# Kernel tuning notes

Hardware: AMD Instinct MI355X
Metric: run time of the kernel (lower is better)

## Reference

```python
import jax, jax.numpy as jnp
import numpy as np

B, N, FEAT, HID, CTX = 16384, 7, 512, 256, 256
COMB = N * HID + CTX  # 2048


def setup_inputs() -> dict:
    key = jax.random.key(0)
    ks = jax.random.split(key, 20)
    s = lambda k, shape, sc=0.05: jax.random.normal(k, shape, dtype=jnp.float32) * sc
    adj = jax.random.randint(ks[1], (N, N), 0, 2).astype(jnp.float32)
    # guarantee self-loops so no row is fully masked (still exercise nan_to_num path robustly)
    adj = jnp.maximum(adj, jnp.eye(N, dtype=jnp.float32))
    return {
        "node_feats": jax.random.normal(ks[0], (B, N, FEAT), dtype=jnp.float32),
        "adj": adj,
        "context": jax.random.normal(ks[2], (B, CTX), dtype=jnp.float32),
        "base_preds": jax.random.normal(ks[3], (B, 5), dtype=jnp.float32),
        "W1": s(ks[4], (HID, FEAT)),
        "a1": s(ks[5], (1, 2 * HID)),
        "W2": s(ks[6], (HID, HID)),
        "a2": s(ks[7], (1, 2 * HID)),
        "wh1_w": s(ks[8], (32, COMB)), "wh1_b": s(ks[9], (32,)),
        "wh2_w": s(ks[10], (16, 32)), "wh2_b": s(ks[11], (16,)),
        "wh3_w": s(ks[12], (5, 16)), "wh3_b": s(ks[13], (5,)),
        "rh1_w": s(ks[14], (16, COMB)), "rh1_b": s(ks[15], (16,)),
        "rh2_w": s(ks[16], (1, 16)), "rh2_b": s(ks[17], (1,)),
    }


def _gat_layer(x, adj, W, a):
    # x: (B, N, in_dim); W: (D, in_dim); a: (1, 2D)
    h = jnp.einsum('bni,di->bnd', x, W)  # (B, N, D)
    D = W.shape[0]
    # a([h_i, h_j]) == h_i @ a[:, :D] + h_j @ a[:, D:]
    s_i = h @ a[0, :D]   # (B, N)
    s_j = h @ a[0, D:]   # (B, N)
    e = s_i[:, :, None] + s_j[:, None, :]          # (B, N, N)
    e = jax.nn.leaky_relu(e, negative_slope=0.2)
    e = jnp.where(adj[None] == 0, -jnp.inf, e)
    alpha = jax.nn.softmax(e, axis=-1)
    alpha = jnp.nan_to_num(alpha, nan=0.0)
    out = jnp.einsum('bij,bjd->bid', alpha, h)     # (B, N, D)
    return out, alpha


def reference(node_feats, adj, context, base_preds, W1, a1, W2, a2,
              wh1_w, wh1_b, wh2_w, wh2_b, wh3_w, wh3_b,
              rh1_w, rh1_b, rh2_w, rh2_b):
    h, _attn1 = _gat_layer(node_feats, adj, W1, a1)
    h = jax.nn.relu(h)
    h, attn2 = _gat_layer(h, adj, W2, a2)
    h = jax.nn.relu(h)
    graph_embed = h.reshape(h.shape[0], -1)                 # (B, N*D)
    combined = jnp.concatenate([graph_embed, context], -1)  # (B, COMB)
    # weight head (dropout is inference-mode identity)
    t = jax.nn.relu(combined @ wh1_w.T + wh1_b)
    t = jax.nn.relu(t @ wh2_w.T + wh2_b)
    raw_weights = t @ wh3_w.T + wh3_b                       # (B, 5)
    weights = jax.nn.softmax(raw_weights, axis=-1)
    weighted_pred = jnp.sum(weights * base_preds, axis=-1)  # (B,)
    r = jnp.tanh(combined @ rh1_w.T + rh1_b)
    residual = (r @ rh2_w.T + rh2_b)[:, 0] * 0.05
    pred = jnp.maximum(weighted_pred + residual, 0.05)
    return pred, weights, attn2
```

## Files before the change

kernel.cpp:

```cpp
#include <hip/hip_runtime.h>

#define B_SZ 16384
#define NN 7
#define HID 256
#define COMB 2048

typedef __attribute__((ext_vector_type(8))) short short8;
typedef __attribute__((ext_vector_type(4))) float floatx4;
typedef __attribute__((ext_vector_type(4))) unsigned short ushortx4;
typedef unsigned short us;

__device__ __forceinline__ float bf2f(us u) {
    union { unsigned int i; float f; } v; v.i = ((unsigned int)u) << 16; return v.f;
}
__device__ __forceinline__ us f2bf(float f) {
    union { unsigned int i; float f; } v; v.f = f;
    return (us)((v.i + 0x7FFFu + ((v.i >> 16) & 1u)) >> 16);
}
__device__ __forceinline__ us f2bf_fast(float f) {
    union { unsigned int i; float f; } v; v.f = f;
    return (us)((v.i + 0x8000u) >> 16);
}

__device__ __forceinline__ int hoff(int r, int k8) {
    return ((r >> 3) << 8) | ((r & 7) << 5) | (k8 & 24) | ((k8 ^ r) & 7);
}
__device__ __forceinline__ int aoff(int r, int k8) {
    return ((r >> 3) << 6) | ((r & 7) << 3) | ((k8 ^ r) & 7);
}

__global__ __launch_bounds__(256) void pack_weights(const float* __restrict__ W1,
                                                    const float* __restrict__ W2,
                                                    const float* __restrict__ wh1,
                                                    const float* __restrict__ rh1,
                                                    us* __restrict__ dst) {
    int i = (blockIdx.x * 256 + threadIdx.x) * 4;
    if (i >= 294912) return;
    const float* src; int off;
    if (i < 131072)      { src = W1;  off = i; }
    else if (i < 196608) { src = W2;  off = i - 131072; }
    else if (i < 262144) { src = wh1; off = i - 196608; }
    else                 { src = rh1; off = i - 262144; }
    floatx4 v = *(const floatx4*)(src + off);
    ushortx4 o = {f2bf(v[0]), f2bf(v[1]), f2bf(v[2]), f2bf(v[3])};
    *(ushortx4*)(dst + i) = o;
}

template <bool WRITE_ALPHA>
__device__ __forceinline__ void attn_graph(us* hs, int r0, const float* adjs, const float* avec,
                                           float* alpha_dst, int lane) {
    const int k8 = lane >> 1, sub = (lane & 1) * 4;
    float hv[NN][4];
#pragma unroll
    for (int n = 0; n < NN; ++n) {
        ushortx4 rr = *(const ushortx4*)(hs + hoff(r0 + n, k8) * 8 + sub);
        hv[n][0] = bf2f(rr[0]); hv[n][1] = bf2f(rr[1]);
        hv[n][2] = bf2f(rr[2]); hv[n][3] = bf2f(rr[3]);
    }
    floatx4 ai = *(const floatx4*)(avec + lane * 4);
    floatx4 aj = *(const floatx4*)(avec + HID + lane * 4);
    float si[NN], sj[NN];
#pragma unroll
    for (int n = 0; n < NN; ++n) {
        float pi = hv[n][0] * ai[0] + hv[n][1] * ai[1] + hv[n][2] * ai[2] + hv[n][3] * ai[3];
        float pj = hv[n][0] * aj[0] + hv[n][1] * aj[1] + hv[n][2] * aj[2] + hv[n][3] * aj[3];
#pragma unroll
        for (int off = 32; off; off >>= 1) {
            pi += __shfl_xor(pi, off);
            pj += __shfl_xor(pj, off);
        }
        si[n] = pi; sj[n] = pj;
    }
    const int j = lane & 7;
    float sjm = sj[0];
    if (j == 1) sjm = sj[1];
    if (j == 2) sjm = sj[2];
    if (j == 3) sjm = sj[3];
    if (j == 4) sjm = sj[4];
    if (j == 5) sjm = sj[5];
    if (j == 6) sjm = sj[6];
    const int jc = (j < 7) ? j : 0;
    float alpha[NN];
#pragma unroll
    for (int i = 0; i < NN; ++i) {
        float x = si[i] + sjm;
        x = (x >= 0.f) ? x : 0.2f * x;
        bool ok = (j < 7) && (adjs[i * 7 + jc] != 0.f);
        float e = ok ? x : -1e30f;
        float m = e;
        m = fmaxf(m, __shfl_xor(m, 1, 8));
        m = fmaxf(m, __shfl_xor(m, 2, 8));
        m = fmaxf(m, __shfl_xor(m, 4, 8));
        float ex = ok ? __expf(e - m) : 0.f;
        float s = ex;
        s += __shfl_xor(s, 1, 8);
        s += __shfl_xor(s, 2, 8);
        s += __shfl_xor(s, 4, 8);
        alpha[i] = (s > 0.f) ? ex * __frcp_rn(s) : 0.f;
    }
    if (WRITE_ALPHA && lane < 7) {
#pragma unroll
        for (int i = 0; i < NN; ++i) alpha_dst[i * NN + lane] = alpha[i];
    }
#pragma unroll
    for (int i = 0; i < NN; ++i) {
        floatx4 o = (floatx4){0.f, 0.f, 0.f, 0.f};
#pragma unroll
        for (int jj = 0; jj < NN; ++jj) {
            float a = __shfl(alpha[i], jj, 8);
            o[0] += a * hv[jj][0]; o[1] += a * hv[jj][1];
            o[2] += a * hv[jj][2]; o[3] += a * hv[jj][3];
        }
        ushortx4 st = {f2bf(fmaxf(o[0], 0.f)), f2bf(fmaxf(o[1], 0.f)),
                       f2bf(fmaxf(o[2], 0.f)), f2bf(fmaxf(o[3], 0.f))};
        *(ushortx4*)(hs + hoff(r0 + i, k8) * 8 + sub) = st;
    }
}

__device__ __forceinline__ void cwrite(us* hs, floatx4 (&acc)[4][2], int wave, int quad, int m16) {
#pragma unroll
    for (int rt = 0; rt < 4; ++rt)
#pragma unroll
        for (int ct = 0; ct < 2; ++ct)
#pragma unroll
            for (int i = 0; i < 4; ++i) {
                int row = rt * 16 + quad * 4 + i;
                if (row < 56)
                    hs[hoff(row, wave * 4 + ct * 2 + (m16 >> 3)) * 8 + (m16 & 7)] =
                        f2bf(acc[rt][ct][i]);
            }
}

__global__ __launch_bounds__(512, 4) void fused_all(
    const float* __restrict__ Af, const us* __restrict__ W1b, const us* __restrict__ W2b,
    const us* __restrict__ Whb, const float* __restrict__ adj, const float* __restrict__ a1v,
    const float* __restrict__ a2v, const float* __restrict__ context,
    const float* __restrict__ wh1_b, const float* __restrict__ wh2_w,
    const float* __restrict__ wh2_b, const float* __restrict__ wh3_w,
    const float* __restrict__ wh3_b, const float* __restrict__ rh1_b,
    const float* __restrict__ rh2_w, const float* __restrict__ rh2_b,
    const float* __restrict__ base_preds, float* __restrict__ out) {
    __shared__ __attribute__((aligned(16))) us hs[16384];
    __shared__ __attribute__((aligned(16))) char ubuf[16384];
    __shared__ float adjs[52];
    us* As = (us*)ubuf;
    float* red = (float*)ubuf;
    float* fin = red + 3072;
    const int tid = threadIdx.x;
    const int wave = tid >> 6, lane = tid & 63;
    const int quad = lane >> 4, m16 = lane & 15;
    const long gbase = (long)blockIdx.x * 8;
    if (tid < 49) adjs[tid] = adj[tid];
    *(ushortx4*)(hs + 14336 + tid * 4) = (ushortx4){0, 0, 0, 0};

    floatx4 acc[4][2];
#pragma unroll
    for (int rt = 0; rt < 4; ++rt)
#pragma unroll
        for (int ct = 0; ct < 2; ++ct) acc[rt][ct] = (floatx4){0.f, 0.f, 0.f, 0.f};

    const int r = tid >> 3, kq8 = tid & 7;
    long rowA = gbase * 7 + r; if (rowA > 114687) rowA = 114687;
    const float* aptr = Af + rowA * 512 + kq8 * 8;
    us* wdst = As + aoff(r, kq8) * 8;
    const int colb = wave * 32;

    floatx4 v0 = *(const floatx4*)aptr;
    floatx4 v1 = *(const floatx4*)(aptr + 4);
#pragma unroll
    for (int s = 0; s < 8; ++s) {
        short8 sv;
        sv[0] = f2bf_fast(v0[0]); sv[1] = f2bf_fast(v0[1]);
        sv[2] = f2bf_fast(v0[2]); sv[3] = f2bf_fast(v0[3]);
        sv[4] = f2bf_fast(v1[0]); sv[5] = f2bf_fast(v1[1]);
        sv[6] = f2bf_fast(v1[2]); sv[7] = f2bf_fast(v1[3]);
        if (s < 7) {
            v0 = *(const floatx4*)(aptr + (s + 1) * 64);
            v1 = *(const floatx4*)(aptr + (s + 1) * 64 + 4);
        }
        *(short8*)(wdst + (s & 1) * 4096) = sv;
        __syncthreads();
        const us* Ab = As + (s & 1) * 4096;
        const int k0 = s * 64;
#pragma unroll
        for (int t = 0; t < 2; ++t) {
            short8 b0 = *(const short8*)(W1b + (long)(colb + m16) * 512 + k0 + t * 32 + quad * 8);
            short8 b1 = *(const short8*)(W1b + (long)(colb + 16 + m16) * 512 + k0 + t * 32 + quad * 8);
            short8 a[4];
#pragma unroll
            for (int rt = 0; rt < 4; ++rt)
                a[rt] = *(const short8*)(Ab + aoff(rt * 16 + m16, t * 4 + quad) * 8);
#pragma unroll
            for (int rt = 0; rt < 4; ++rt) {
                acc[rt][0] = __builtin_amdgcn_mfma_f32_16x16x32_bf16(a[rt], b0, acc[rt][0], 0, 0, 0);
                acc[rt][1] = __builtin_amdgcn_mfma_f32_16x16x32_bf16(a[rt], b1, acc[rt][1], 0, 0, 0);
            }
        }
    }
    cwrite(hs, acc, wave, quad, m16);
    __syncthreads();
    attn_graph<false>(hs, wave * NN, adjs, a1v, nullptr, lane);
    __syncthreads();

#pragma unroll
    for (int rt = 0; rt < 4; ++rt)
#pragma unroll
        for (int ct = 0; ct < 2; ++ct) acc[rt][ct] = (floatx4){0.f, 0.f, 0.f, 0.f};
#pragma unroll
    for (int s = 0; s < 4; ++s) {
        const int k0 = s * 64;
#pragma unroll
        for (int t = 0; t < 2; ++t) {
            short8 b0 = *(const short8*)(W2b + (long)(colb + m16) * 256 + k0 + t * 32 + quad * 8);
            short8 b1 = *(const short8*)(W2b + (long)(colb + 16 + m16) * 256 + k0 + t * 32 + quad * 8);
            short8 a[4];
#pragma unroll
            for (int rt = 0; rt < 4; ++rt)
                a[rt] = *(const short8*)(hs + hoff(rt * 16 + m16, s * 8 + t * 4 + quad) * 8);
#pragma unroll
            for (int rt = 0; rt < 4; ++rt) {
                acc[rt][0] = __builtin_amdgcn_mfma_f32_16x16x32_bf16(a[rt], b0, acc[rt][0], 0, 0, 0);
                acc[rt][1] = __builtin_amdgcn_mfma_f32_16x16x32_bf16(a[rt], b1, acc[rt][1], 0, 0, 0);
            }
        }
    }
    __syncthreads();
    cwrite(hs, acc, wave, quad, m16);
    __syncthreads();
    attn_graph<true>(hs, wave * NN, adjs, a2v, out + 6 * B_SZ + (gbase + wave) * 49, lane);
    __syncthreads();

    floatx4 acc3[3];
#pragma unroll
    for (int ct = 0; ct < 3; ++ct) acc3[ct] = (floatx4){0.f, 0.f, 0.f, 0.f};
    const int g = m16 & 7;
#pragma unroll
    for (int s2 = 0; s2 < 8; ++s2) {
        const int kk = s2 * 32;
        short8 a;
        if (wave < 7) {
            a = *(const short8*)(hs + hoff(g * NN + wave, s2 * 4 + quad) * 8);
        } else {
            const float* cp = context + (gbase + g) * 256 + kk + quad * 8;
            floatx4 c0 = *(const floatx4*)cp;
            floatx4 c1 = *(const floatx4*)(cp + 4);
            a[0] = (short)f2bf(c0[0]); a[1] = (short)f2bf(c0[1]);
            a[2] = (short)f2bf(c0[2]); a[3] = (short)f2bf(c0[3]);
            a[4] = (short)f2bf(c1[0]); a[5] = (short)f2bf(c1[1]);
            a[6] = (short)f2bf(c1[2]); a[7] = (short)f2bf(c1[3]);
        }
#pragma unroll
        for (int ct = 0; ct < 3; ++ct) {
            short8 bh = *(const short8*)(Whb + (long)(ct * 16 + m16) * COMB + wave * 256 + kk + quad * 8);
            acc3[ct] = __builtin_amdgcn_mfma_f32_16x16x32_bf16(a, bh, acc3[ct], 0, 0, 0);
        }
    }
#pragma unroll
    for (int ct = 0; ct < 3; ++ct)
#pragma unroll
        for (int i = 0; i < 4; ++i) {
            int g2 = quad * 4 + i;
            if (g2 < 8) red[wave * 384 + g2 * 48 + ct * 16 + m16] = acc3[ct][i];
        }
    __syncthreads();
    if (tid < 384) {
        float ssum = 0.f;
#pragma unroll
        for (int w = 0; w < 8; ++w) ssum += red[w * 384 + tid];
        fin[tid] = ssum;
    }
    __syncthreads();

    const int fj = lane & 7, fg = lane >> 3;
    const long fb = gbase + fg;
    float rp = 0.f;
    float* t1s = red;
    float* t2s = red + 256;
    if (tid < 64) {
        const float* g48 = fin + fg * 48;
#pragma unroll
        for (int x = 0; x < 4; ++x) {
            int k = fj * 4 + x;
            t1s[fg * 32 + k] = fmaxf(g48[k] + wh1_b[k], 0.f);
        }
#pragma unroll
        for (int x = 0; x < 2; ++x) {
            int k = fj * 2 + x;
            float rv = tanhf(g48[32 + k] + rh1_b[k]);
            rp += rh2_w[k] * rv;
        }
    }
    __syncthreads();
    if (tid < 64) {
        float s0 = wh2_b[fj * 2], s1 = wh2_b[fj * 2 + 1];
#pragma unroll
        for (int k = 0; k < 32; ++k) {
            float tv = t1s[fg * 32 + k];
            s0 += wh2_w[(fj * 2) * 32 + k] * tv;
            s1 += wh2_w[(fj * 2 + 1) * 32 + k] * tv;
        }
        t2s[fg * 16 + fj * 2] = fmaxf(s0, 0.f);
        t2s[fg * 16 + fj * 2 + 1] = fmaxf(s1, 0.f);
    }
    __syncthreads();
    if (tid < 64) {
        float rw = -1e30f;
        if (fj < 5) {
            float s = wh3_b[fj];
#pragma unroll
            for (int k = 0; k < 16; ++k) s += wh3_w[fj * 16 + k] * t2s[fg * 16 + k];
            rw = s;
        }
        float m = rw;
        m = fmaxf(m, __shfl_xor(m, 1, 8));
        m = fmaxf(m, __shfl_xor(m, 2, 8));
        m = fmaxf(m, __shfl_xor(m, 4, 8));
        float e = (fj < 5) ? __expf(rw - m) : 0.f;
        float se = e;
        se += __shfl_xor(se, 1, 8);
        se += __shfl_xor(se, 2, 8);
        se += __shfl_xor(se, 4, 8);
        float inv = 1.f / se;
        float wp = 0.f;
        if (fj < 5) {
            float w = e * inv;
            out[B_SZ + fb * 5 + fj] = w;
            wp = w * base_preds[fb * 5 + fj];
        }
        wp += __shfl_xor(wp, 1, 8);
        wp += __shfl_xor(wp, 2, 8);
        wp += __shfl_xor(wp, 4, 8);
        float rs = rp;
        rs += __shfl_xor(rs, 1, 8);
        rs += __shfl_xor(rs, 2, 8);
        rs += __shfl_xor(rs, 4, 8);
        if (fj == 0) out[fb] = fmaxf(wp + (rs + rh2_b[0]) * 0.05f, 0.05f);
    }
}

extern "C" void kernel_launch(void* const* d_in, const int* in_sizes, int n_in,
                              void* d_out, int out_size, void* d_ws, size_t ws_size,
                              hipStream_t stream) {
    const float* node_feats = (const float*)d_in[0];
    const float* adj        = (const float*)d_in[1];
    const float* context    = (const float*)d_in[2];
    const float* base_preds = (const float*)d_in[3];
    const float* W1         = (const float*)d_in[4];
    const float* a1         = (const float*)d_in[5];
    const float* W2         = (const float*)d_in[6];
    const float* a2         = (const float*)d_in[7];
    const float* wh1_w = (const float*)d_in[8];
    const float* wh1_b = (const float*)d_in[9];
    const float* wh2_w = (const float*)d_in[10];
    const float* wh2_b = (const float*)d_in[11];
    const float* wh3_w = (const float*)d_in[12];
    const float* wh3_b = (const float*)d_in[13];
    const float* rh1_w = (const float*)d_in[14];
    const float* rh1_b = (const float*)d_in[15];
    const float* rh2_w = (const float*)d_in[16];
    const float* rh2_b = (const float*)d_in[17];
    float* out = (float*)d_out;

    char* ws = (char*)d_ws;
    us* W1b = (us*)ws;
    us* W2b = W1b + 131072;
    us* Whb = W2b + 65536;

    pack_weights<<<288, 256, 0, stream>>>(W1, W2, wh1_w, rh1_w, W1b);

    fused_all<<<2048, 512, 0, stream>>>(node_feats, W1b, W2b, Whb, adj, a1, a2, context,
                                        wh1_b, wh2_w, wh2_b, wh3_w, wh3_b,
                                        rh1_b, rh2_w, rh2_b, base_preds, out);
}
```

Baseline: 523.7 us.

## Halve graphs per block to 4, doubling grid and shrinking LDS tiles

Each block now handles 4 graphs (28 rows, padded to 32) instead of 8 (56 rows, padded to 64). The grid doubles to 4096 blocks, shared memory per block halves, and the A tile loads and MFMA row tiles shrink to match. The aim is cheaper per-block work and more resident blocks. In exchange, every block streams the W1/W2/head weights from cache for half as many rows, and only half the waves do useful attention or final-head work.

```diff
diff --git a/kernel.cpp b/kernel.cpp
--- a/kernel.cpp
+++ b/kernel.cpp
@@ -23,10 +23,10 @@
 }
 
 __device__ __forceinline__ int hoff(int r, int k8) {
-    return ((r >> 3) << 8) | ((r & 7) << 5) | (k8 & 24) | ((k8 ^ r) & 7);
+    return (r << 5) | (k8 & 24) | ((k8 ^ r) & 7);
 }
 __device__ __forceinline__ int aoff(int r, int k8) {
-    return ((r >> 3) << 6) | ((r & 7) << 3) | ((k8 ^ r) & 7);
+    return (r << 3) | ((k8 ^ r) & 7);
 }
 
 __global__ __launch_bounds__(256) void pack_weights(const float* __restrict__ W1,
@@ -117,15 +117,15 @@
     }
 }
 
-__device__ __forceinline__ void cwrite(us* hs, floatx4 (&acc)[4][2], int wave, int quad, int m16) {
-#pragma unroll
-    for (int rt = 0; rt < 4; ++rt)
+__device__ __forceinline__ void cwrite(us* hs, floatx4 (&acc)[2][2], int wave, int quad, int m16) {
+#pragma unroll
+    for (int rt = 0; rt < 2; ++rt)
 #pragma unroll
         for (int ct = 0; ct < 2; ++ct)
 #pragma unroll
             for (int i = 0; i < 4; ++i) {
                 int row = rt * 16 + quad * 4 + i;
-                if (row < 56)
+                if (row < 28)
                     hs[hoff(row, wave * 4 + ct * 2 + (m16 >> 3)) * 8 + (m16 & 7)] =
                         f2bf(acc[rt][ct][i]);
             }
@@ -140,118 +140,111 @@
     const float* __restrict__ wh3_b, const float* __restrict__ rh1_b,
     const float* __restrict__ rh2_w, const float* __restrict__ rh2_b,
     const float* __restrict__ base_preds, float* __restrict__ out) {
-    __shared__ __attribute__((aligned(16))) us hs[16384];
-    __shared__ __attribute__((aligned(16))) char ubuf[16384];
+    __shared__ __attribute__((aligned(16))) us hs[8192];
+    __shared__ __attribute__((aligned(16))) char ubuf[8192];
     __shared__ float adjs[52];
     us* As = (us*)ubuf;
     float* red = (float*)ubuf;
-    float* fin = red + 3072;
+    float* fin = red + 1536;
     const int tid = threadIdx.x;
     const int wave = tid >> 6, lane = tid & 63;
     const int quad = lane >> 4, m16 = lane & 15;
-    const long gbase = (long)blockIdx.x * 8;
+    const long gbase = (long)blockIdx.x * 4;
     if (tid < 49) adjs[tid] = adj[tid];
-    *(ushortx4*)(hs + 14336 + tid * 4) = (ushortx4){0, 0, 0, 0};
-
-    floatx4 acc[4][2];
-#pragma unroll
-    for (int rt = 0; rt < 4; ++rt)
+    *(unsigned int*)&hs[7168 + tid * 2] = 0u;
+
+    floatx4 acc[2][2];
+#pragma unroll
+    for (int rt = 0; rt < 2; ++rt)
 #pragma unroll
         for (int ct = 0; ct < 2; ++ct) acc[rt][ct] = (floatx4){0.f, 0.f, 0.f, 0.f};
 
-    const int r = tid >> 3, kq8 = tid & 7;
+    const int r = tid >> 4, kq4 = tid & 15;
     long rowA = gbase * 7 + r; if (rowA > 114687) rowA = 114687;
-    const float* aptr = Af + rowA * 512 + kq8 * 8;
-    us* wdst = As + aoff(r, kq8) * 8;
+    const float* aptr = Af + rowA * 512 + kq4 * 4;
+    us* wdst = As + aoff(r, kq4 >> 1) * 8 + (kq4 & 1) * 4;
     const int colb = wave * 32;
-
-    floatx4 v0 = *(const floatx4*)aptr;
-    floatx4 v1 = *(const floatx4*)(aptr + 4);
+    const us* w1p0 = W1b + (colb + m16) * 512 + quad * 8;
+    const us* w1p1 = w1p0 + 16 * 512;
+
+    floatx4 v = *(const floatx4*)aptr;
 #pragma unroll
     for (int s = 0; s < 8; ++s) {
-        short8 sv;
-        sv[0] = f2bf_fast(v0[0]); sv[1] = f2bf_fast(v0[1]);
-        sv[2] = f2bf_fast(v0[2]); sv[3] = f2bf_fast(v0[3]);
-        sv[4] = f2bf_fast(v1[0]); sv[5] = f2bf_fast(v1[1]);
-        sv[6] = f2bf_fast(v1[2]); sv[7] = f2bf_fast(v1[3]);
-        if (s < 7) {
-            v0 = *(const floatx4*)(aptr + (s + 1) * 64);
-            v1 = *(const floatx4*)(aptr + (s + 1) * 64 + 4);
-        }
-        *(short8*)(wdst + (s & 1) * 4096) = sv;
+        ushortx4 sv = {f2bf_fast(v[0]), f2bf_fast(v[1]), f2bf_fast(v[2]), f2bf_fast(v[3])};
+        if (s < 7) v = *(const floatx4*)(aptr + (s + 1) * 64);
+        *(ushortx4*)(wdst + (s & 1) * 2048) = sv;
         __syncthreads();
-        const us* Ab = As + (s & 1) * 4096;
+        const us* Ab = As + (s & 1) * 2048;
         const int k0 = s * 64;
 #pragma unroll
         for (int t = 0; t < 2; ++t) {
-            short8 b0 = *(const short8*)(W1b + (long)(colb + m16) * 512 + k0 + t * 32 + quad * 8);
-            short8 b1 = *(const short8*)(W1b + (long)(colb + 16 + m16) * 512 + k0 + t * 32 + quad * 8);
-            short8 a[4];
-#pragma unroll
-            for (int rt = 0; rt < 4; ++rt)
-                a[rt] = *(const short8*)(Ab + aoff(rt * 16 + m16, t * 4 + quad) * 8);
-#pragma unroll
-            for (int rt = 0; rt < 4; ++rt) {
-                acc[rt][0] = __builtin_amdgcn_mfma_f32_16x16x32_bf16(a[rt], b0, acc[rt][0], 0, 0, 0);
-                acc[rt][1] = __builtin_amdgcn_mfma_f32_16x16x32_bf16(a[rt], b1, acc[rt][1], 0, 0, 0);
-            }
+            short8 b0 = *(const short8*)(w1p0 + k0 + t * 32);
+            short8 b1 = *(const short8*)(w1p1 + k0 + t * 32);
+            short8 a0 = *(const short8*)(Ab + aoff(m16, t * 4 + quad) * 8);
+            short8 a1 = *(const short8*)(Ab + aoff(16 + m16, t * 4 + quad) * 8);
+            acc[0][0] = __builtin_amdgcn_mfma_f32_16x16x32_bf16(a0, b0, acc[0][0], 0, 0, 0);
+            acc[0][1] = __builtin_amdgcn_mfma_f32_16x16x32_bf16(a0, b1, acc[0][1], 0, 0, 0);
+            acc[1][0] = __builtin_amdgcn_mfma_f32_16x16x32_bf16(a1, b0, acc[1][0], 0, 0, 0);
+            acc[1][1] = __builtin_amdgcn_mfma_f32_16x16x32_bf16(a1, b1, acc[1][1], 0, 0, 0);
         }
     }
     cwrite(hs, acc, wave, quad, m16);
     __syncthreads();
-    attn_graph<false>(hs, wave * NN, adjs, a1v, nullptr, lane);
-    __syncthreads();
-
-#pragma unroll
-    for (int rt = 0; rt < 4; ++rt)
+    if (wave < 4) attn_graph<false>(hs, wave * NN, adjs, a1v, nullptr, lane);
+    __syncthreads();
+
+#pragma unroll
+    for (int rt = 0; rt < 2; ++rt)
 #pragma unroll
         for (int ct = 0; ct < 2; ++ct) acc[rt][ct] = (floatx4){0.f, 0.f, 0.f, 0.f};
+    const us* w2p0 = W2b + (colb + m16) * 256 + quad * 8;
+    const us* w2p1 = w2p0 + 16 * 256;
 #pragma unroll
     for (int s = 0; s < 4; ++s) {
-        const int k0 = s * 64;
 #pragma unroll
         for (int t = 0; t < 2; ++t) {
-            short8 b0 = *(const short8*)(W2b + (long)(colb + m16) * 256 + k0 + t * 32 + quad * 8);
-            short8 b1 = *(const short8*)(W2b + (long)(colb + 16 + m16) * 256 + k0 + t * 32 + quad * 8);
-            short8 a[4];
-#pragma unroll
-            for (int rt = 0; rt < 4; ++rt)
-                a[rt] = *(const short8*)(hs + hoff(rt * 16 + m16, s * 8 + t * 4 + quad) * 8);
-#pragma unroll
-            for (int rt = 0; rt < 4; ++rt) {
-                acc[rt][0] = __builtin_amdgcn_mfma_f32_16x16x32_bf16(a[rt], b0, acc[rt][0], 0, 0, 0);
-                acc[rt][1] = __builtin_amdgcn_mfma_f32_16x16x32_bf16(a[rt], b1, acc[rt][1], 0, 0, 0);
-            }
+            short8 b0 = *(const short8*)(w2p0 + s * 64 + t * 32);
+            short8 b1 = *(const short8*)(w2p1 + s * 64 + t * 32);
+            short8 a0 = *(const short8*)(hs + hoff(m16, s * 8 + t * 4 + quad) * 8);
+            short8 a1 = *(const short8*)(hs + hoff(16 + m16, s * 8 + t * 4 + quad) * 8);
+            acc[0][0] = __builtin_amdgcn_mfma_f32_16x16x32_bf16(a0, b0, acc[0][0], 0, 0, 0);
+            acc[0][1] = __builtin_amdgcn_mfma_f32_16x16x32_bf16(a0, b1, acc[0][1], 0, 0, 0);
+            acc[1][0] = __builtin_amdgcn_mfma_f32_16x16x32_bf16(a1, b0, acc[1][0], 0, 0, 0);
+            acc[1][1] = __builtin_amdgcn_mfma_f32_16x16x32_bf16(a1, b1, acc[1][1], 0, 0, 0);
         }
     }
     __syncthreads();
     cwrite(hs, acc, wave, quad, m16);
     __syncthreads();
-    attn_graph<true>(hs, wave * NN, adjs, a2v, out + 6 * B_SZ + (gbase + wave) * 49, lane);
+    if (wave < 4) attn_graph<true>(hs, wave * NN, adjs, a2v,
+                                   out + 6 * B_SZ + (gbase + wave) * 49, lane);
     __syncthreads();
 
     floatx4 acc3[3];
 #pragma unroll
     for (int ct = 0; ct < 3; ++ct) acc3[ct] = (floatx4){0.f, 0.f, 0.f, 0.f};
-    const int g = m16 & 7;
 #pragma unroll
     for (int s2 = 0; s2 < 8; ++s2) {
-        const int kk = s2 * 32;
         short8 a;
         if (wave < 7) {
-            a = *(const short8*)(hs + hoff(g * NN + wave, s2 * 4 + quad) * 8);
+            int row = (m16 < 4) ? (m16 * NN + wave) : 28;
+            a = *(const short8*)(hs + hoff(row, s2 * 4 + quad) * 8);
         } else {
-            const float* cp = context + (gbase + g) * 256 + kk + quad * 8;
-            floatx4 c0 = *(const floatx4*)cp;
-            floatx4 c1 = *(const floatx4*)(cp + 4);
-            a[0] = (short)f2bf(c0[0]); a[1] = (short)f2bf(c0[1]);
-            a[2] = (short)f2bf(c0[2]); a[3] = (short)f2bf(c0[3]);
-            a[4] = (short)f2bf(c1[0]); a[5] = (short)f2bf(c1[1]);
-            a[6] = (short)f2bf(c1[2]); a[7] = (short)f2bf(c1[3]);
+            if (m16 < 4) {
+                const float* cp = context + (gbase + m16) * 256 + s2 * 32 + quad * 8;
+                floatx4 c0 = *(const floatx4*)cp;
+                floatx4 c1 = *(const floatx4*)(cp + 4);
+                a[0] = (short)f2bf(c0[0]); a[1] = (short)f2bf(c0[1]);
+                a[2] = (short)f2bf(c0[2]); a[3] = (short)f2bf(c0[3]);
+                a[4] = (short)f2bf(c1[0]); a[5] = (short)f2bf(c1[1]);
+                a[6] = (short)f2bf(c1[2]); a[7] = (short)f2bf(c1[3]);
+            } else {
+                a = (short8){0, 0, 0, 0, 0, 0, 0, 0};
+            }
         }
 #pragma unroll
         for (int ct = 0; ct < 3; ++ct) {
-            short8 bh = *(const short8*)(Whb + (long)(ct * 16 + m16) * COMB + wave * 256 + kk + quad * 8);
+            short8 bh = *(const short8*)(Whb + (long)(ct * 16 + m16) * COMB + wave * 256 + s2 * 32 + quad * 8);
             acc3[ct] = __builtin_amdgcn_mfma_f32_16x16x32_bf16(a, bh, acc3[ct], 0, 0, 0);
         }
     }
@@ -260,23 +253,23 @@
 #pragma unroll
         for (int i = 0; i < 4; ++i) {
             int g2 = quad * 4 + i;
-            if (g2 < 8) red[wave * 384 + g2 * 48 + ct * 16 + m16] = acc3[ct][i];
-        }
-    __syncthreads();
-    if (tid < 384) {
+            if (g2 < 4) red[wave * 192 + g2 * 48 + ct * 16 + m16] = acc3[ct][i];
+        }
+    __syncthreads();
+    if (tid < 192) {
         float ssum = 0.f;
 #pragma unroll
-        for (int w = 0; w < 8; ++w) ssum += red[w * 384 + tid];
+        for (int w = 0; w < 8; ++w) ssum += red[w * 192 + tid];
         fin[tid] = ssum;
     }
     __syncthreads();
 
-    const int fj = lane & 7, fg = lane >> 3;
+    const int fj = tid & 7, fg = (tid >> 3) & 3;
     const long fb = gbase + fg;
     float rp = 0.f;
     float* t1s = red;
-    float* t2s = red + 256;
-    if (tid < 64) {
+    float* t2s = red + 128;
+    if (tid < 32) {
         const float* g48 = fin + fg * 48;
 #pragma unroll
         for (int x = 0; x < 4; ++x) {
@@ -291,7 +284,7 @@
         }
     }
     __syncthreads();
-    if (tid < 64) {
+    if (tid < 32) {
         float s0 = wh2_b[fj * 2], s1 = wh2_b[fj * 2 + 1];
 #pragma unroll
         for (int k = 0; k < 32; ++k) {
@@ -303,7 +296,7 @@
         t2s[fg * 16 + fj * 2 + 1] = fmaxf(s1, 0.f);
     }
     __syncthreads();
-    if (tid < 64) {
+    if (tid < 32) {
         float rw = -1e30f;
         if (fj < 5) {
             float s = wh3_b[fj];
@@ -368,7 +361,7 @@
 
     pack_weights<<<288, 256, 0, stream>>>(W1, W2, wh1_w, rh1_w, W1b);
 
-    fused_all<<<2048, 512, 0, stream>>>(node_feats, W1b, W2b, Whb, adj, a1, a2, context,
+    fused_all<<<4096, 512, 0, stream>>>(node_feats, W1b, W2b, Whb, adj, a1, a2, context,
                                         wh1_b, wh2_w, wh2_b, wh3_w, wh3_b,
                                         rh1_b, rh2_w, rh2_b, base_preds, out);
 }
```

Measured after the change: 672.4 us. 1.28x slower.

## Retile GEMMs to 2x4 wave grid and load node features directly into registers

Applied to the files above, without the earlier changes.

The first GEMM no longer stages node features through a double-buffered LDS tile with a barrier every k-step. Each wave now reads its own fp32 A rows from global memory, converts them to bf16 in registers and feeds the MFMAs directly. The wave layout changes from 8 column slices covering all 64 rows to a 2 (row halves) by 4 (column quarters) grid, so each wave owns 32 rows by 64 columns. This halves A reuse per wave but raises B reuse and removes the LDS staging and per-step syncs. Global A loads are now less coalesced (16-row by 8-float fragments) and redundant across the four column waves, relying on cache.

```diff
diff --git a/kernel.cpp b/kernel.cpp
--- a/kernel.cpp
+++ b/kernel.cpp
@@ -21,12 +21,17 @@
     union { unsigned int i; float f; } v; v.f = f;
     return (us)((v.i + 0x8000u) >> 16);
 }
+__device__ __forceinline__ short8 pack8(floatx4 u0, floatx4 u1) {
+    short8 a;
+    a[0] = f2bf_fast(u0[0]); a[1] = f2bf_fast(u0[1]);
+    a[2] = f2bf_fast(u0[2]); a[3] = f2bf_fast(u0[3]);
+    a[4] = f2bf_fast(u1[0]); a[5] = f2bf_fast(u1[1]);
+    a[6] = f2bf_fast(u1[2]); a[7] = f2bf_fast(u1[3]);
+    return a;
+}
 
 __device__ __forceinline__ int hoff(int r, int k8) {
     return ((r >> 3) << 8) | ((r & 7) << 5) | (k8 & 24) | ((k8 ^ r) & 7);
-}
-__device__ __forceinline__ int aoff(int r, int k8) {
-    return ((r >> 3) << 6) | ((r & 7) << 3) | ((k8 ^ r) & 7);
 }
 
 __global__ __launch_bounds__(256) void pack_weights(const float* __restrict__ W1,
@@ -117,16 +122,17 @@
     }
 }
 
-__device__ __forceinline__ void cwrite(us* hs, floatx4 (&acc)[4][2], int wave, int quad, int m16) {
-#pragma unroll
-    for (int rt = 0; rt < 4; ++rt)
-#pragma unroll
-        for (int ct = 0; ct < 2; ++ct)
+__device__ __forceinline__ void cwrite(us* hs, floatx4 (&acc)[2][4], int rh, int cq,
+                                       int quad, int m16) {
+#pragma unroll
+    for (int rt = 0; rt < 2; ++rt)
+#pragma unroll
+        for (int ct = 0; ct < 4; ++ct)
 #pragma unroll
             for (int i = 0; i < 4; ++i) {
-                int row = rt * 16 + quad * 4 + i;
+                int row = rh * 32 + rt * 16 + quad * 4 + i;
                 if (row < 56)
-                    hs[hoff(row, wave * 4 + ct * 2 + (m16 >> 3)) * 8 + (m16 & 7)] =
+                    hs[hoff(row, cq * 8 + ct * 2 + (m16 >> 3)) * 8 + (m16 & 7)] =
                         f2bf(acc[rt][ct][i]);
             }
 }
@@ -141,93 +147,79 @@
     const float* __restrict__ rh2_w, const float* __restrict__ rh2_b,
     const float* __restrict__ base_preds, float* __restrict__ out) {
     __shared__ __attribute__((aligned(16))) us hs[16384];
-    __shared__ __attribute__((aligned(16))) char ubuf[16384];
+    __shared__ float red[8 * 384];
+    __shared__ float fin[384];
     __shared__ float adjs[52];
-    us* As = (us*)ubuf;
-    float* red = (float*)ubuf;
-    float* fin = red + 3072;
     const int tid = threadIdx.x;
     const int wave = tid >> 6, lane = tid & 63;
     const int quad = lane >> 4, m16 = lane & 15;
+    const int rh = wave >> 2, cq = wave & 3;
     const long gbase = (long)blockIdx.x * 8;
+    const long rowBase = (long)blockIdx.x * 56;
     if (tid < 49) adjs[tid] = adj[tid];
     *(ushortx4*)(hs + 14336 + tid * 4) = (ushortx4){0, 0, 0, 0};
 
-    floatx4 acc[4][2];
-#pragma unroll
-    for (int rt = 0; rt < 4; ++rt)
-#pragma unroll
-        for (int ct = 0; ct < 2; ++ct) acc[rt][ct] = (floatx4){0.f, 0.f, 0.f, 0.f};
-
-    const int r = tid >> 3, kq8 = tid & 7;
-    long rowA = gbase * 7 + r; if (rowA > 114687) rowA = 114687;
-    const float* aptr = Af + rowA * 512 + kq8 * 8;
-    us* wdst = As + aoff(r, kq8) * 8;
-    const int colb = wave * 32;
-
-    floatx4 v0 = *(const floatx4*)aptr;
-    floatx4 v1 = *(const floatx4*)(aptr + 4);
-#pragma unroll
-    for (int s = 0; s < 8; ++s) {
-        short8 sv;
-        sv[0] = f2bf_fast(v0[0]); sv[1] = f2bf_fast(v0[1]);
-        sv[2] = f2bf_fast(v0[2]); sv[3] = f2bf_fast(v0[3]);
-        sv[4] = f2bf_fast(v1[0]); sv[5] = f2bf_fast(v1[1]);
-        sv[6] = f2bf_fast(v1[2]); sv[7] = f2bf_fast(v1[3]);
-        if (s < 7) {
-            v0 = *(const floatx4*)(aptr + (s + 1) * 64);
-            v1 = *(const floatx4*)(aptr + (s + 1) * 64 + 4);
-        }
-        *(short8*)(wdst + (s & 1) * 4096) = sv;
-        __syncthreads();
-        const us* Ab = As + (s & 1) * 4096;
-        const int k0 = s * 64;
-#pragma unroll
-        for (int t = 0; t < 2; ++t) {
-            short8 b0 = *(const short8*)(W1b + (long)(colb + m16) * 512 + k0 + t * 32 + quad * 8);
-            short8 b1 = *(const short8*)(W1b + (long)(colb + 16 + m16) * 512 + k0 + t * 32 + quad * 8);
-            short8 a[4];
-#pragma unroll
-            for (int rt = 0; rt < 4; ++rt)
-                a[rt] = *(const short8*)(Ab + aoff(rt * 16 + m16, t * 4 + quad) * 8);
-#pragma unroll
-            for (int rt = 0; rt < 4; ++rt) {
-                acc[rt][0] = __builtin_amdgcn_mfma_f32_16x16x32_bf16(a[rt], b0, acc[rt][0], 0, 0, 0);
-                acc[rt][1] = __builtin_amdgcn_mfma_f32_16x16x32_bf16(a[rt], b1, acc[rt][1], 0, 0, 0);
-            }
-        }
-    }
-    cwrite(hs, acc, wave, quad, m16);
+    floatx4 acc[2][4];
+#pragma unroll
+    for (int rt = 0; rt < 2; ++rt)
+#pragma unroll
+        for (int ct = 0; ct < 4; ++ct) acc[rt][ct] = (floatx4){0.f, 0.f, 0.f, 0.f};
+
+    const float* ap0; const float* ap1;
+    {
+        long r0 = rowBase + rh * 32 + m16;      if (r0 > 114687) r0 = 114687;
+        long r1 = rowBase + rh * 32 + 16 + m16; if (r1 > 114687) r1 = 114687;
+        ap0 = Af + r0 * 512 + quad * 8;
+        ap1 = Af + r1 * 512 + quad * 8;
+    }
+    const us* w1p = W1b + (cq * 64 + m16) * 512 + quad * 8;
+#pragma unroll 2
+    for (int ks = 0; ks < 16; ++ks) {
+        const int ko = ks * 32;
+        floatx4 u0 = *(const floatx4*)(ap0 + ko);
+        floatx4 u1 = *(const floatx4*)(ap0 + ko + 4);
+        floatx4 u2 = *(const floatx4*)(ap1 + ko);
+        floatx4 u3 = *(const floatx4*)(ap1 + ko + 4);
+        short8 b[4];
+#pragma unroll
+        for (int ct = 0; ct < 4; ++ct) b[ct] = *(const short8*)(w1p + ct * 16 * 512 + ko);
+        short8 a0 = pack8(u0, u1);
+        short8 a1 = pack8(u2, u3);
+#pragma unroll
+        for (int ct = 0; ct < 4; ++ct) {
+            acc[0][ct] = __builtin_amdgcn_mfma_f32_16x16x32_bf16(a0, b[ct], acc[0][ct], 0, 0, 0);
+            acc[1][ct] = __builtin_amdgcn_mfma_f32_16x16x32_bf16(a1, b[ct], acc[1][ct], 0, 0, 0);
+        }
+    }
+    cwrite(hs, acc, rh, cq, quad, m16);
     __syncthreads();
     attn_graph<false>(hs, wave * NN, adjs, a1v, nullptr, lane);
     __syncthreads();
 
 #pragma unroll
-    for (int rt = 0; rt < 4; ++rt)
-#pragma unroll
-        for (int ct = 0; ct < 2; ++ct) acc[rt][ct] = (floatx4){0.f, 0.f, 0.f, 0.f};
-#pragma unroll
-    for (int s = 0; s < 4; ++s) {
-        const int k0 = s * 64;
-#pragma unroll
-        for (int t = 0; t < 2; ++t) {
-            short8 b0 = *(const short8*)(W2b + (long)(colb + m16) * 256 + k0 + t * 32 + quad * 8);
-            short8 b1 = *(const short8*)(W2b + (long)(colb + 16 + m16) * 256 + k0 + t * 32 + quad * 8);
-            short8 a[4];
-#pragma unroll
-            for (int rt = 0; rt < 4; ++rt)
-                a[rt] = *(const short8*)(hs + hoff(rt * 16 + m16, s * 8 + t * 4 + quad) * 8);
-#pragma unroll
-            for (int rt = 0; rt < 4; ++rt) {
-                acc[rt][0] = __builtin_amdgcn_mfma_f32_16x16x32_bf16(a[rt], b0, acc[rt][0], 0, 0, 0);
-                acc[rt][1] = __builtin_amdgcn_mfma_f32_16x16x32_bf16(a[rt], b1, acc[rt][1], 0, 0, 0);
-            }
-        }
-    }
-    __syncthreads();
-    cwrite(hs, acc, wave, quad, m16);
-    __syncthreads();
-    attn_graph<true>(hs, wave * NN, adjs, a2v, out + 6 * B_SZ + (gbase + wave) * 49, lane);
+    for (int rt = 0; rt < 2; ++rt)
+#pragma unroll
+        for (int ct = 0; ct < 4; ++ct) acc[rt][ct] = (floatx4){0.f, 0.f, 0.f, 0.f};
+    const us* w2p = W2b + (cq * 64 + m16) * 256 + quad * 8;
+#pragma unroll 2
+    for (int ks = 0; ks < 8; ++ks) {
+        const int ko = ks * 32;
+        short8 a0 = *(const short8*)(hs + hoff(rh * 32 + m16, ks * 4 + quad) * 8);
+        short8 a1 = *(const short8*)(hs + hoff(rh * 32 + 16 + m16, ks * 4 + quad) * 8);
+        short8 b[4];
+#pragma unroll
+        for (int ct = 0; ct < 4; ++ct) b[ct] = *(const short8*)(w2p + ct * 16 * 256 + ko);
+#pragma unroll
+        for (int ct = 0; ct < 4; ++ct) {
+            acc[0][ct] = __builtin_amdgcn_mfma_f32_16x16x32_bf16(a0, b[ct], acc[0][ct], 0, 0, 0);
+            acc[1][ct] = __builtin_amdgcn_mfma_f32_16x16x32_bf16(a1, b[ct], acc[1][ct], 0, 0, 0);
+        }
+    }
+    __syncthreads();
+    cwrite(hs, acc, rh, cq, quad, m16);
+    __syncthreads();
+    attn_graph<true>(hs, wave * NN, adjs, a2v,
+                     out + 6 * B_SZ + (gbase + wave) * 49, lane);
     __syncthreads();
 
     floatx4 acc3[3];
```

Result: slower. 683.9 us (+30.6%).

## Fold attention score vectors into GEMM via precomputed W^T·a columns

Applied to the files above, without the earlier changes.

Precomputes W1^T·a1 and W2^T·a2 as extra bf16 weight rows in a small new kernel, so the attention scores s_i and s_j come out of an extra MFMA inside each projection GEMM. That replaces the per-node cross-wave dot products and shuffle reductions in the attention step. Softmax is now computed per lane across all 7 neighbours, removing the segmented shuffles for max, sum and broadcasting alpha. It costs one extra MFMA per k-step for the waves that hold score rows, plus a small extra launch, and scores are now taken from bf16 inputs and bf16 folded weights instead of the rounded h.

```diff
diff --git a/kernel.cpp b/kernel.cpp
--- a/kernel.cpp
+++ b/kernel.cpp
@@ -46,71 +46,76 @@
     *(ushortx4*)(dst + i) = o;
 }
 
+__global__ __launch_bounds__(256) void pack_scores(const float* __restrict__ W1,
+                                                   const float* __restrict__ a1,
+                                                   const float* __restrict__ W2,
+                                                   const float* __restrict__ a2,
+                                                   us* __restrict__ Wsc1,
+                                                   us* __restrict__ Wsc2) {
+    int t = blockIdx.x * 256 + threadIdx.x;
+    if (t < 512) {
+        float s0 = 0.f, s1 = 0.f;
+        for (int d = 0; d < 256; ++d) {
+            float w = W1[d * 512 + t];
+            s0 += a1[d] * w; s1 += a1[256 + d] * w;
+        }
+        Wsc1[t] = f2bf(s0); Wsc1[512 + t] = f2bf(s1);
+        for (int r = 2; r < 16; ++r) Wsc1[r * 512 + t] = 0;
+    } else if (t < 768) {
+        int k = t - 512;
+        float s0 = 0.f, s1 = 0.f;
+        for (int d = 0; d < 256; ++d) {
+            float w = W2[d * 256 + k];
+            s0 += a2[d] * w; s1 += a2[256 + d] * w;
+        }
+        Wsc2[k] = f2bf(s0); Wsc2[256 + k] = f2bf(s1);
+        for (int r = 2; r < 16; ++r) Wsc2[r * 256 + k] = 0;
+    }
+}
+
 template <bool WRITE_ALPHA>
-__device__ __forceinline__ void attn_graph(us* hs, int r0, const float* adjs, const float* avec,
+__device__ __forceinline__ void attn_graph(us* hs, int r0, const float* sc, const float* adjs,
                                            float* alpha_dst, int lane) {
     const int k8 = lane >> 1, sub = (lane & 1) * 4;
-    float hv[NN][4];
+    const int j = lane & 7;
+    floatx4 hv[NN];
 #pragma unroll
     for (int n = 0; n < NN; ++n) {
         ushortx4 rr = *(const ushortx4*)(hs + hoff(r0 + n, k8) * 8 + sub);
-        hv[n][0] = bf2f(rr[0]); hv[n][1] = bf2f(rr[1]);
-        hv[n][2] = bf2f(rr[2]); hv[n][3] = bf2f(rr[3]);
-    }
-    floatx4 ai = *(const floatx4*)(avec + lane * 4);
-    floatx4 aj = *(const floatx4*)(avec + HID + lane * 4);
-    float si[NN], sj[NN];
-#pragma unroll
-    for (int n = 0; n < NN; ++n) {
-        float pi = hv[n][0] * ai[0] + hv[n][1] * ai[1] + hv[n][2] * ai[2] + hv[n][3] * ai[3];
-        float pj = hv[n][0] * aj[0] + hv[n][1] * aj[1] + hv[n][2] * aj[2] + hv[n][3] * aj[3];
-#pragma unroll
-        for (int off = 32; off; off >>= 1) {
-            pi += __shfl_xor(pi, off);
-            pj += __shfl_xor(pj, off);
-        }
-        si[n] = pi; sj[n] = pj;
-    }
-    const int j = lane & 7;
-    float sjm = sj[0];
-    if (j == 1) sjm = sj[1];
-    if (j == 2) sjm = sj[2];
-    if (j == 3) sjm = sj[3];
-    if (j == 4) sjm = sj[4];
-    if (j == 5) sjm = sj[5];
-    if (j == 6) sjm = sj[6];
-    const int jc = (j < 7) ? j : 0;
-    float alpha[NN];
+        hv[n] = (floatx4){bf2f(rr[0]), bf2f(rr[1]), bf2f(rr[2]), bf2f(rr[3])};
+    }
+    float sjv[NN];
+#pragma unroll
+    for (int n = 0; n < NN; ++n) sjv[n] = sc[(r0 + n) * 2 + 1];
 #pragma unroll
     for (int i = 0; i < NN; ++i) {
-        float x = si[i] + sjm;
-        x = (x >= 0.f) ? x : 0.2f * x;
-        bool ok = (j < 7) && (adjs[i * 7 + jc] != 0.f);
-        float e = ok ? x : -1e30f;
-        float m = e;
-        m = fmaxf(m, __shfl_xor(m, 1, 8));
-        m = fmaxf(m, __shfl_xor(m, 2, 8));
-        m = fmaxf(m, __shfl_xor(m, 4, 8));
-        float ex = ok ? __expf(e - m) : 0.f;
-        float s = ex;
-        s += __shfl_xor(s, 1, 8);
-        s += __shfl_xor(s, 2, 8);
-        s += __shfl_xor(s, 4, 8);
-        alpha[i] = (s > 0.f) ? ex * __frcp_rn(s) : 0.f;
-    }
-    if (WRITE_ALPHA && lane < 7) {
-#pragma unroll
-        for (int i = 0; i < NN; ++i) alpha_dst[i * NN + lane] = alpha[i];
-    }
-#pragma unroll
-    for (int i = 0; i < NN; ++i) {
+        const float siv = sc[(r0 + i) * 2];
+        float ex[NN];
+        float m = -1e30f;
+#pragma unroll
+        for (int jj = 0; jj < NN; ++jj) {
+            float x = siv + sjv[jj];
+            x = (x >= 0.f) ? x : 0.2f * x;
+            ex[jj] = (adjs[i * 7 + jj] != 0.f) ? x : -1e30f;
+            m = fmaxf(m, ex[jj]);
+        }
+        float sum = 0.f;
+#pragma unroll
+        for (int jj = 0; jj < NN; ++jj) {
+            float e2 = __expf(ex[jj] - m);
+            ex[jj] = e2; sum += e2;
+        }
+        const float inv = (sum > 0.f) ? __frcp_rn(sum) : 0.f;
         floatx4 o = (floatx4){0.f, 0.f, 0.f, 0.f};
+        float mya = 0.f;
 #pragma unroll
         for (int jj = 0; jj < NN; ++jj) {
-            float a = __shfl(alpha[i], jj, 8);
+            float a = ex[jj] * inv;
+            if (jj == j) mya = a;
             o[0] += a * hv[jj][0]; o[1] += a * hv[jj][1];
             o[2] += a * hv[jj][2]; o[3] += a * hv[jj][3];
         }
+        if (WRITE_ALPHA && lane < 7) alpha_dst[i * NN + lane] = mya;
         ushortx4 st = {f2bf(fmaxf(o[0], 0.f)), f2bf(fmaxf(o[1], 0.f)),
                        f2bf(fmaxf(o[2], 0.f)), f2bf(fmaxf(o[3], 0.f))};
         *(ushortx4*)(hs + hoff(r0 + i, k8) * 8 + sub) = st;
@@ -133,8 +138,8 @@
 
 __global__ __launch_bounds__(512, 4) void fused_all(
     const float* __restrict__ Af, const us* __restrict__ W1b, const us* __restrict__ W2b,
-    const us* __restrict__ Whb, const float* __restrict__ adj, const float* __restrict__ a1v,
-    const float* __restrict__ a2v, const float* __restrict__ context,
+    const us* __restrict__ Whb, const us* __restrict__ Wsc1, const us* __restrict__ Wsc2,
+    const float* __restrict__ adj, const float* __restrict__ context,
     const float* __restrict__ wh1_b, const float* __restrict__ wh2_w,
     const float* __restrict__ wh2_b, const float* __restrict__ wh3_w,
     const float* __restrict__ wh3_b, const float* __restrict__ rh1_b,
@@ -142,6 +147,7 @@
     const float* __restrict__ base_preds, float* __restrict__ out) {
     __shared__ __attribute__((aligned(16))) us hs[16384];
     __shared__ __attribute__((aligned(16))) char ubuf[16384];
+    __shared__ float scA[128];
     __shared__ float adjs[52];
     us* As = (us*)ubuf;
     float* red = (float*)ubuf;
@@ -149,6 +155,7 @@
     const int tid = threadIdx.x;
     const int wave = tid >> 6, lane = tid & 63;
     const int quad = lane >> 4, m16 = lane & 15;
+    const int rsel = wave & 3;
     const long gbase = (long)blockIdx.x * 8;
     if (tid < 49) adjs[tid] = adj[tid];
     *(ushortx4*)(hs + 14336 + tid * 4) = (ushortx4){0, 0, 0, 0};
@@ -158,6 +165,7 @@
     for (int rt = 0; rt < 4; ++rt)
 #pragma unroll
         for (int ct = 0; ct < 2; ++ct) acc[rt][ct] = (floatx4){0.f, 0.f, 0.f, 0.f};
+    floatx4 accs = (floatx4){0.f, 0.f, 0.f, 0.f};
 
     const int r = tid >> 3, kq8 = tid & 7;
     long rowA = gbase * 7 + r; if (rowA > 114687) rowA = 114687;
@@ -186,6 +194,7 @@
         for (int t = 0; t < 2; ++t) {
             short8 b0 = *(const short8*)(W1b + (long)(colb + m16) * 512 + k0 + t * 32 + quad * 8);
             short8 b1 = *(const short8*)(W1b + (long)(colb + 16 + m16) * 512 + k0 + t * 32 + quad * 8);
+            short8 bs = *(const short8*)(Wsc1 + m16 * 512 + k0 + t * 32 + quad * 8);
             short8 a[4];
 #pragma unroll
             for (int rt = 0; rt < 4; ++rt)
@@ -194,18 +203,25 @@
             for (int rt = 0; rt < 4; ++rt) {
                 acc[rt][0] = __builtin_amdgcn_mfma_f32_16x16x32_bf16(a[rt], b0, acc[rt][0], 0, 0, 0);
                 acc[rt][1] = __builtin_amdgcn_mfma_f32_16x16x32_bf16(a[rt], b1, acc[rt][1], 0, 0, 0);
+                if (rt == rsel)
+                    accs = __builtin_amdgcn_mfma_f32_16x16x32_bf16(a[rt], bs, accs, 0, 0, 0);
             }
         }
     }
     cwrite(hs, acc, wave, quad, m16);
-    __syncthreads();
-    attn_graph<false>(hs, wave * NN, adjs, a1v, nullptr, lane);
+    if (wave < 4 && m16 < 2) {
+#pragma unroll
+        for (int i = 0; i < 4; ++i) scA[(rsel * 16 + quad * 4 + i) * 2 + m16] = accs[i];
+    }
+    __syncthreads();
+    attn_graph<false>(hs, wave * NN, scA, adjs, nullptr, lane);
     __syncthreads();
 
 #pragma unroll
     for (int rt = 0; rt < 4; ++rt)
 #pragma unroll
         for (int ct = 0; ct < 2; ++ct) acc[rt][ct] = (floatx4){0.f, 0.f, 0.f, 0.f};
+    accs = (floatx4){0.f, 0.f, 0.f, 0.f};
 #pragma unroll
     for (int s = 0; s < 4; ++s) {
         const int k0 = s * 64;
@@ -213,6 +229,7 @@
         for (int t = 0; t < 2; ++t) {
             short8 b0 = *(const short8*)(W2b + (long)(colb + m16) * 256 + k0 + t * 32 + quad * 8);
             short8 b1 = *(const short8*)(W2b + (long)(colb + 16 + m16) * 256 + k0 + t * 32 + quad * 8);
+            short8 bs = *(const short8*)(Wsc2 + m16 * 256 + k0 + t * 32 + quad * 8);
             short8 a[4];
 #pragma unroll
             for (int rt = 0; rt < 4; ++rt)
@@ -221,13 +238,20 @@
             for (int rt = 0; rt < 4; ++rt) {
                 acc[rt][0] = __builtin_amdgcn_mfma_f32_16x16x32_bf16(a[rt], b0, acc[rt][0], 0, 0, 0);
                 acc[rt][1] = __builtin_amdgcn_mfma_f32_16x16x32_bf16(a[rt], b1, acc[rt][1], 0, 0, 0);
+                if (rt == rsel)
+                    accs = __builtin_amdgcn_mfma_f32_16x16x32_bf16(a[rt], bs, accs, 0, 0, 0);
             }
         }
     }
     __syncthreads();
     cwrite(hs, acc, wave, quad, m16);
-    __syncthreads();
-    attn_graph<true>(hs, wave * NN, adjs, a2v, out + 6 * B_SZ + (gbase + wave) * 49, lane);
+    if (wave < 4 && m16 < 2) {
+#pragma unroll
+        for (int i = 0; i < 4; ++i) scA[(rsel * 16 + quad * 4 + i) * 2 + m16] = accs[i];
+    }
+    __syncthreads();
+    attn_graph<true>(hs, wave * NN, scA, adjs,
+                     out + 6 * B_SZ + (gbase + wave) * 49, lane);
     __syncthreads();
 
     floatx4 acc3[3];
@@ -362,13 +386,16 @@
     float* out = (float*)d_out;
 
     char* ws = (char*)d_ws;
-    us* W1b = (us*)ws;
-    us* W2b = W1b + 131072;
-    us* Whb = W2b + 65536;
+    us* W1b  = (us*)ws;
+    us* W2b  = W1b + 131072;
+    us* Whb  = W2b + 65536;
+    us* Wsc1 = Whb + 98304;
+    us* Wsc2 = Wsc1 + 8192;
 
     pack_weights<<<288, 256, 0, stream>>>(W1, W2, wh1_w, rh1_w, W1b);
-
-    fused_all<<<2048, 512, 0, stream>>>(node_feats, W1b, W2b, Whb, adj, a1, a2, context,
+    pack_scores<<<3, 256, 0, stream>>>(W1, a1, W2, a2, Wsc1, Wsc2);
+
+    fused_all<<<2048, 512, 0, stream>>>(node_feats, W1b, W2b, Whb, Wsc1, Wsc2, adj, context,
                                         wh1_b, wh2_w, wh2_b, wh3_w, wh3_b,
                                         rh1_b, rh2_w, rh2_b, base_preds, out);
 }
```

New measurement: 579.4 us. 10.7% more time.
